# Kernel tuning notes

Hardware: AMD Instinct MI355X
Metric: run time of the kernel (lower is better)

Reference implementation:

```python
import jax, jax.numpy as jnp
import numpy as np

K = 4
TEMP = 0.5
PAD = 1

def setup_inputs() -> dict:
    key = jax.random.key(0)
    ks = jax.random.split(key, 5)
    B, C, H, W = 32, 256, 64, 64
    O, HID = 256, 65  # int(256*0.25)+1
    x = jax.random.normal(ks[0], (B, C, H, W), dtype=jnp.float32)
    w1 = jax.random.normal(ks[1], (HID, C), dtype=jnp.float32) * 0.05
    w2 = jax.random.normal(ks[2], (K * O, HID), dtype=jnp.float32) * 0.05
    b2 = jnp.zeros((K * O,), dtype=jnp.float32)
    weight = jax.random.normal(ks[3], (K, O, C, 3, 3), dtype=jnp.float32) * 0.05
    return {"x": x, "w1": w1, "w2": w2, "b2": b2, "weight": weight}

def _dyn_conv(x, w1, w2, b2, weight):
    B, C, H, W = x.shape
    Kk, O = weight.shape[0], weight.shape[1]
    # GPM2d attention: global avg pool -> 1x1 conv -> relu -> 1x1 conv -> softmax over K
    pooled = jnp.mean(x, axis=(2, 3))                     # [B, C]
    h = jax.nn.relu(pooled @ w1.T)                        # [B, HID]
    logits = (h @ w2.T + b2).reshape(B, Kk, O)            # [B, K, O]
    attn = jax.nn.softmax(logits / TEMP, axis=1)          # softmax over K experts
    # aggregate per-sample, per-out-channel weights: [B, O, C, k, k]
    agg_w = jnp.einsum('bko,kocij->bocij', attn, weight)
    # per-sample conv (equivalent to groups=batch trick in torch)
    def conv1(xi, wi):
        return jax.lax.conv_general_dilated(
            xi[None], wi, window_strides=(1, 1),
            padding=[(PAD, PAD), (PAD, PAD)],
            dimension_numbers=('NCHW', 'OIHW', 'NCHW'))[0]
    return jax.vmap(conv1)(x, agg_w)                      # [B, O, H, W]

def reference(x, w1, w2, b2, weight):
    return _dyn_conv(x, w1, w2, b2, weight)
```

## Files before the change

### kernel.cpp

```cpp
#include <hip/hip_runtime.h>
#include <stdint.h>

typedef unsigned short ushort_t;
typedef __attribute__((ext_vector_type(8))) short short8;
typedef __attribute__((ext_vector_type(8))) unsigned short ushortx8;
typedef __attribute__((ext_vector_type(4))) float floatx4;

#define B_    32
#define C_    256
#define O_    256
#define HID_  65
#define HW_   4096
#define KDIM  2304
#define XP_H  66
#define XPAD_ELEMS ((size_t)B_ * XP_H * XP_H * C_)
#define WAGG_ELEMS ((size_t)B_ * O_ * KDIM)

static __device__ __forceinline__ unsigned short f2bf(float f) {
  unsigned u = __float_as_uint(f);
  u += 0x7fffu + ((u >> 16) & 1u);
  return (unsigned short)(u >> 16);
}

static __device__ __forceinline__ void gld_lds16(const void* g, void* l) {
  __builtin_amdgcn_global_load_lds((__attribute__((address_space(1))) void*)(g),
                                   (__attribute__((address_space(3))) void*)(l),
                                   16, 0, 0);
}

__global__ void pad_kernel(const float* __restrict__ x, ushort_t* __restrict__ xpad,
                           float* __restrict__ partial) {
  __shared__ float tileT[64][65];
  __shared__ float pool[4][64];
  const int hwT = blockIdx.x, cT = blockIdx.y, b = blockIdx.z;
  const int t = threadIdx.x;
  const int hw0 = hwT * 64, c0 = cT * 64;
  const float* src = x + ((size_t)(b * C_ + c0)) * HW_ + hw0;

  if (cT == 0) {
    const int tid = hwT * 256 + t;
    if (tid < 8320) {
      uint4 z = {0u, 0u, 0u, 0u};
      uint4* base = (uint4*)(xpad + (size_t)b * XP_H * XP_H * C_);
      size_t idx;
      if (tid < 2112) idx = (size_t)tid;
      else if (tid < 4224) idx = (size_t)65 * 2112 + (tid - 2112);
      else if (tid < 6272) {
        const int i = tid - 4224;
        idx = (size_t)(1 + (i >> 5)) * 2112 + (i & 31);
      } else {
        const int i = tid - 6272;
        idx = (size_t)(1 + (i >> 5)) * 2112 + 65 * 32 + (i & 31);
      }
      base[idx] = z;
    }
  }

#pragma unroll
  for (int p = 0; p < 4; ++p) {
    const int flat = p * 256 + t;
    const int c = flat >> 4, h4 = (flat & 15) * 4;
    const float4 v = *(const float4*)(src + (size_t)c * HW_ + h4);
    tileT[h4 + 0][c] = v.x;
    tileT[h4 + 1][c] = v.y;
    tileT[h4 + 2][c] = v.z;
    tileT[h4 + 3][c] = v.w;
  }
  __syncthreads();

  {
    const int c = t & 63, qh = t >> 6;
    float s = 0.f;
#pragma unroll
    for (int i = 0; i < 16; ++i) s += tileT[qh * 16 + i][c];
    pool[qh][c] = s;
  }
  __syncthreads();
  if (t < 64) {
    partial[(size_t)hwT * (B_ * C_) + b * C_ + c0 + t] =
        pool[0][t] + pool[1][t] + pool[2][t] + pool[3][t];
  }

#pragma unroll
  for (int p = 0; p < 2; ++p) {
    const int flat = p * 256 + t;
    const int hw = flat >> 3, cg = (flat & 7) * 8;
    ushortx8 v;
#pragma unroll
    for (int j = 0; j < 8; ++j) v[j] = f2bf(tileT[hw][cg + j]);
    const int h = (hw0 + hw) >> 6, w = (hw0 + hw) & 63;
    *(ushortx8*)(xpad + (((size_t)b * XP_H + (h + 1)) * XP_H + (w + 1)) * C_ + c0 + cg) = v;
  }
}

__global__ void attn_kernel(const float* __restrict__ partial,
                            const float* __restrict__ w1,
                            const float* __restrict__ w2,
                            const float* __restrict__ b2,
                            float* __restrict__ attn) {
  __shared__ float sp[C_];
  __shared__ float sh[HID_];
  const int b = blockIdx.x, t = threadIdx.x;
  {
    float s = 0.f;
#pragma unroll
    for (int i = 0; i < 64; ++i) s += partial[(size_t)i * (B_ * C_) + b * C_ + t];
    sp[t] = s * (1.f / 4096.f);
  }
  __syncthreads();
  if (t < HID_) {
    float a = 0.f;
    for (int c = 0; c < C_; ++c) a += sp[c] * w1[t * C_ + c];
    sh[t] = fmaxf(a, 0.f);
  }
  __syncthreads();
  float lg[4];
#pragma unroll
  for (int k = 0; k < 4; ++k) {
    float a = b2[k * O_ + t];
    for (int j = 0; j < HID_; ++j) a += sh[j] * w2[(k * O_ + t) * HID_ + j];
    lg[k] = a * 2.0f;
  }
  float mx = fmaxf(fmaxf(lg[0], lg[1]), fmaxf(lg[2], lg[3]));
  float e0 = expf(lg[0] - mx), e1 = expf(lg[1] - mx);
  float e2 = expf(lg[2] - mx), e3 = expf(lg[3] - mx);
  float inv = 1.f / (e0 + e1 + e2 + e3);
  attn[(b * 4 + 0) * O_ + t] = e0 * inv;
  attn[(b * 4 + 1) * O_ + t] = e1 * inv;
  attn[(b * 4 + 2) * O_ + t] = e2 * inv;
  attn[(b * 4 + 3) * O_ + t] = e3 * inv;
}

__global__ void agg_kernel(const float* __restrict__ attn,
                           const float* __restrict__ wt,
                           ushort_t* __restrict__ wagg) {
  const int o = blockIdx.x;
  const int b0 = blockIdx.y * 4;
  const int t = threadIdx.x;
  float wr[4][9];
#pragma unroll
  for (int k = 0; k < 4; ++k) {
    const float* src = wt + (size_t)(k * O_ + o) * KDIM + t * 9;
#pragma unroll
    for (int n = 0; n < 9; ++n) wr[k][n] = src[n];
  }
#pragma unroll
  for (int bi = 0; bi < 4; ++bi) {
    const int b = b0 + bi;
    const float a0 = attn[(b * 4 + 0) * O_ + o];
    const float a1 = attn[(b * 4 + 1) * O_ + o];
    const float a2 = attn[(b * 4 + 2) * O_ + o];
    const float a3 = attn[(b * 4 + 3) * O_ + o];
    ushort_t* dst = wagg + (size_t)(b * O_ + o) * KDIM;
#pragma unroll
    for (int n = 0; n < 9; ++n) {
      float v = a0 * wr[0][n] + a1 * wr[1][n] + a2 * wr[2][n] + a3 * wr[3][n];
      dst[n * C_ + t] = f2bf(v);
    }
  }
}

__global__ __launch_bounds__(512) void gemm_kernel(const ushort_t* __restrict__ xpad,
                                                   const ushort_t* __restrict__ wagg,
                                                   float* __restrict__ out) {
  __shared__ short lA0[2 * 256 * 64];
  __shared__ short lB0[2 * 256 * 64];

  const int bid = blockIdx.x;
  const int xcd = bid & 7;
  const int q   = bid >> 3;
  const int b   = xcd + ((q >> 4) << 3);
  const int hwT = q & 15;
  const int hwBase = hwT << 8;
  const int h0     = hwT << 2;

  const int t    = threadIdx.x;
  const int lane = t & 63;
  const int wv   = t >> 6;

  const int rS  = lane >> 3;
  const int pS  = lane & 7;
  const int lch = pS ^ rS;
  size_t aG[4], bG[4];
  int ldsOff[4];
#pragma unroll
  for (int j = 0; j < 4; ++j) {
    const int row = wv * 32 + j * 8 + rS;
    aG[j] = (size_t)(b * O_ + row) * KDIM + lch * 8;
    const int hl = row >> 6, wl2 = row & 63;
    bG[j] = ((size_t)(b * XP_H + h0 + hl) * XP_H + wl2) * C_ + lch * 8;
    ldsOff[j] = (wv * 32 + j * 8) * 64;
  }

  const int lm   = lane & 15;
  const int quad = lane >> 4;
  const int wr   = wv >> 2;
  const int wc   = wv & 3;
  const int mW   = wr << 7;
  const int nW   = wc << 6;
  int aBase[2], bBase[2];
#pragma unroll
  for (int h = 0; h < 2; ++h) {
    const int ps = ((h * 4 + quad) ^ (lm & 7)) * 8;
    aBase[h] = (mW + lm) * 64 + ps;
    bBase[h] = (nW + lm) * 64 + ps;
  }

  floatx4 acc[8][4] = {};

#pragma unroll
  for (int j = 0; j < 4; ++j) {
    gld_lds16(wagg + aG[j], lA0 + ldsOff[j]);
    gld_lds16(xpad + bG[j], lB0 + ldsOff[j]);
  }
#pragma unroll
  for (int j = 0; j < 4; ++j) {
    gld_lds16(wagg + aG[j] + 64, lA0 + 16384 + ldsOff[j]);
    gld_lds16(xpad + bG[j] + 64, lB0 + 16384 + ldsOff[j]);
  }
  __builtin_amdgcn_s_waitcnt(0x0f78);
  __builtin_amdgcn_s_barrier();
  __builtin_amdgcn_sched_barrier(0);

#pragma unroll 1
  for (int tt = 0; tt < 36; ++tt) {
    const int cb = (tt & 1) * 16384;
    const short* bufA = lA0 + cb;
    const short* bufB = lB0 + cb;
#pragma unroll
    for (int h = 0; h < 2; ++h) {
      short8 af[8], bf[4];
#pragma unroll
      for (int i = 0; i < 8; ++i) af[i] = *(const short8*)(bufA + aBase[h] + i * 1024);
#pragma unroll
      for (int i = 0; i < 4; ++i) bf[i] = *(const short8*)(bufB + bBase[h] + i * 1024);
      __builtin_amdgcn_s_setprio(1);
#pragma unroll
      for (int mi = 0; mi < 8; ++mi)
#pragma unroll
        for (int ni = 0; ni < 4; ++ni)
          acc[mi][ni] = __builtin_amdgcn_mfma_f32_16x16x32_bf16(
              af[mi], bf[ni], acc[mi][ni], 0, 0, 0);
      __builtin_amdgcn_s_setprio(0);
    }
    if (tt == 35) break;
    __builtin_amdgcn_sched_barrier(0);
    __builtin_amdgcn_s_barrier();
    if (tt + 2 < 36) {
      const int kt  = tt + 2;
      const int tap = kt >> 2;
      const size_t aK = (size_t)kt << 6;
      const size_t bK = (size_t)((tap / 3) * XP_H + (tap % 3)) * C_ + ((kt & 3) << 6);
      short* dA = lA0 + cb;
      short* dB = lB0 + cb;
#pragma unroll
      for (int j = 0; j < 4; ++j) {
        gld_lds16(wagg + aG[j] + aK, dA + ldsOff[j]);
        gld_lds16(xpad + bG[j] + bK, dB + ldsOff[j]);
      }
      __builtin_amdgcn_s_waitcnt(0x0f78);
    } else {
      __builtin_amdgcn_s_waitcnt(0x0f70);
    }
    __builtin_amdgcn_s_barrier();
    __builtin_amdgcn_sched_barrier(0);
  }

  const size_t outBase = (size_t)b * O_ * HW_;
#pragma unroll
  for (int mi = 0; mi < 8; ++mi) {
#pragma unroll
    for (int ni = 0; ni < 4; ++ni) {
      const int hw = hwBase + nW + ni * 16 + lm;
#pragma unroll
      for (int r = 0; r < 4; ++r) {
        const int o = mW + mi * 16 + quad * 4 + r;
        out[outBase + (size_t)o * HW_ + hw] = acc[mi][ni][r];
      }
    }
  }
}

extern "C" void kernel_launch(void* const* d_in, const int* in_sizes, int n_in,
                              void* d_out, int out_size, void* d_ws, size_t ws_size,
                              hipStream_t stream) {
  const float* x  = (const float*)d_in[0];
  const float* w1 = (const float*)d_in[1];
  const float* w2 = (const float*)d_in[2];
  const float* b2 = (const float*)d_in[3];
  const float* wt = (const float*)d_in[4];
  float* out = (float*)d_out;

  char* ws = (char*)d_ws;
  ushort_t* xpad = (ushort_t*)ws;
  ushort_t* wagg = (ushort_t*)(ws + XPAD_ELEMS * 2);
  float* partial = (float*)(ws + XPAD_ELEMS * 2 + WAGG_ELEMS * 2);
  float* attn    = partial + 64 * B_ * C_;

  pad_kernel<<<dim3(64, 4, B_), 256, 0, stream>>>(x, xpad, partial);
  attn_kernel<<<B_, 256, 0, stream>>>(partial, w1, w2, b2, attn);
  agg_kernel<<<dim3(O_, 8), 256, 0, stream>>>(attn, wt, wagg);
  gemm_kernel<<<512, 512, 0, stream>>>(xpad, wagg, out);
}
```

Baseline: 428.5 us.

## Split main GEMM loop into four barrier-phased MFMA stages with staggered prefetch

Restructures the conv GEMM K-loop into four sub-phases, each loading half the A fragments from LDS and then running 16 MFMAs, with barriers between phases. Global-to-LDS loads for the next tiles are spread across phases: part of A for tt+1 early, the rest of A and all of B for tt+2 later. The staging row mapping is also remapped. The goal is to overlap LDS reads and global loads with MFMA work in a ping-pong style and to cut register pressure from 12 fragments to 8. The cost is many more barriers per iteration and more complex waitcnt accounting, which raises the risk of stalls or hazards.

```diff
diff --git a/kernel.cpp b/kernel.cpp
--- a/kernel.cpp
+++ b/kernel.cpp
@@ -27,6 +27,10 @@
                                    (__attribute__((address_space(3))) void*)(l),
                                    16, 0, 0);
 }
+
+#define FENCE() __builtin_amdgcn_sched_barrier(0)
+#define BAR()   __builtin_amdgcn_s_barrier()
+#define LGKM0() __builtin_amdgcn_s_waitcnt(0xC07F)
 
 __global__ void pad_kernel(const float* __restrict__ x, ushort_t* __restrict__ xpad,
                            float* __restrict__ partial) {
@@ -181,23 +185,20 @@
   const int rS  = lane >> 3;
   const int pS  = lane & 7;
   const int lch = pS ^ rS;
-  size_t aG[4], bG[4];
-  int ldsOff[4];
+  size_t aG2[4], bG2[4];
+  int sOff[4];
 #pragma unroll
   for (int j = 0; j < 4; ++j) {
-    const int row = wv * 32 + j * 8 + rS;
-    aG[j] = (size_t)(b * O_ + row) * KDIM + lch * 8;
-    const int hl = row >> 6, wl2 = row & 63;
-    bG[j] = ((size_t)(b * XP_H + h0 + hl) * XP_H + wl2) * C_ + lch * 8;
-    ldsOff[j] = (wv * 32 + j * 8) * 64;
+    const int row = j * 64 + wv * 8 + rS;
+    aG2[j] = (size_t)(b * O_ + row) * KDIM + lch * 8;
+    bG2[j] = ((size_t)(b * XP_H + h0 + j) * XP_H + (wv * 8 + rS)) * C_ + lch * 8;
+    sOff[j] = (j * 64 + wv * 8) * 64;
   }
 
   const int lm   = lane & 15;
   const int quad = lane >> 4;
-  const int wr   = wv >> 2;
-  const int wc   = wv & 3;
-  const int mW   = wr << 7;
-  const int nW   = wc << 6;
+  const int mW   = (wv >> 2) << 7;
+  const int nW   = (wv & 3) << 6;
   int aBase[2], bBase[2];
 #pragma unroll
   for (int h = 0; h < 2; ++h) {
@@ -206,64 +207,102 @@
     bBase[h] = (nW + lm) * 64 + ps;
   }
 
+  auto stageA = [&](int j, int kt, short* dst) {
+    gld_lds16(wagg + aG2[j] + ((size_t)kt << 6), dst + sOff[j]);
+  };
+  auto stageB = [&](int j, int kt, short* dst) {
+    const int tap = kt >> 2;
+    const size_t off = (size_t)((tap / 3) * XP_H + (tap % 3)) * C_ + ((kt & 3) << 6);
+    gld_lds16(xpad + bG2[j] + off, dst + sOff[j]);
+  };
+
   floatx4 acc[8][4] = {};
 
 #pragma unroll
   for (int j = 0; j < 4; ++j) {
-    gld_lds16(wagg + aG[j], lA0 + ldsOff[j]);
-    gld_lds16(xpad + bG[j], lB0 + ldsOff[j]);
-  }
-#pragma unroll
-  for (int j = 0; j < 4; ++j) {
-    gld_lds16(wagg + aG[j] + 64, lA0 + 16384 + ldsOff[j]);
-    gld_lds16(xpad + bG[j] + 64, lB0 + 16384 + ldsOff[j]);
-  }
-  __builtin_amdgcn_s_waitcnt(0x0f78);
-  __builtin_amdgcn_s_barrier();
-  __builtin_amdgcn_sched_barrier(0);
+    stageA(j, 0, lA0);
+    stageB(j, 0, lB0);
+  }
+  stageA(0, 1, lA0 + 16384);
+  stageA(2, 1, lA0 + 16384);
+#pragma unroll
+  for (int j = 0; j < 4; ++j) stageB(j, 1, lB0 + 16384);
+  __builtin_amdgcn_s_waitcnt(0x0f76);
+  BAR();
+  FENCE();
 
 #pragma unroll 1
   for (int tt = 0; tt < 36; ++tt) {
-    const int cb = (tt & 1) * 16384;
+    const int cb = (tt & 1) << 14;
     const short* bufA = lA0 + cb;
     const short* bufB = lB0 + cb;
-#pragma unroll
-    for (int h = 0; h < 2; ++h) {
-      short8 af[8], bf[4];
-#pragma unroll
-      for (int i = 0; i < 8; ++i) af[i] = *(const short8*)(bufA + aBase[h] + i * 1024);
-#pragma unroll
-      for (int i = 0; i < 4; ++i) bf[i] = *(const short8*)(bufB + bBase[h] + i * 1024);
-      __builtin_amdgcn_s_setprio(1);
-#pragma unroll
-      for (int mi = 0; mi < 8; ++mi)
-#pragma unroll
-        for (int ni = 0; ni < 4; ++ni)
-          acc[mi][ni] = __builtin_amdgcn_mfma_f32_16x16x32_bf16(
-              af[mi], bf[ni], acc[mi][ni], 0, 0, 0);
-      __builtin_amdgcn_s_setprio(0);
-    }
-    if (tt == 35) break;
-    __builtin_amdgcn_sched_barrier(0);
-    __builtin_amdgcn_s_barrier();
-    if (tt + 2 < 36) {
-      const int kt  = tt + 2;
-      const int tap = kt >> 2;
-      const size_t aK = (size_t)kt << 6;
-      const size_t bK = (size_t)((tap / 3) * XP_H + (tap % 3)) * C_ + ((kt & 3) << 6);
-      short* dA = lA0 + cb;
-      short* dB = lB0 + cb;
-#pragma unroll
-      for (int j = 0; j < 4; ++j) {
-        gld_lds16(wagg + aG[j] + aK, dA + ldsOff[j]);
-        gld_lds16(xpad + bG[j] + bK, dB + ldsOff[j]);
-      }
-      __builtin_amdgcn_s_waitcnt(0x0f78);
-    } else {
-      __builtin_amdgcn_s_waitcnt(0x0f70);
-    }
-    __builtin_amdgcn_s_barrier();
-    __builtin_amdgcn_sched_barrier(0);
+    short* oA = lA0 + (cb ^ 16384);
+    short8 af[4], bf[4];
+
+#pragma unroll
+    for (int i = 0; i < 4; ++i) af[i] = *(const short8*)(bufA + aBase[0] + i * 1024);
+#pragma unroll
+    for (int i = 0; i < 4; ++i) bf[i] = *(const short8*)(bufB + bBase[0] + i * 1024);
+    if (tt < 35) {
+      stageA(1, tt + 1, oA);
+      stageA(3, tt + 1, oA);
+    }
+    FENCE(); BAR(); LGKM0(); FENCE();
+    __builtin_amdgcn_s_setprio(1);
+#pragma unroll
+    for (int mi = 0; mi < 4; ++mi)
+#pragma unroll
+      for (int ni = 0; ni < 4; ++ni)
+        acc[mi][ni] = __builtin_amdgcn_mfma_f32_16x16x32_bf16(af[mi], bf[ni], acc[mi][ni], 0, 0, 0);
+    __builtin_amdgcn_s_setprio(0);
+    FENCE(); BAR(); FENCE();
+
+#pragma unroll
+    for (int i = 0; i < 4; ++i) af[i] = *(const short8*)(bufA + aBase[0] + (4 + i) * 1024);
+    FENCE(); BAR(); LGKM0(); FENCE();
+    __builtin_amdgcn_s_setprio(1);
+#pragma unroll
+    for (int mi = 0; mi < 4; ++mi)
+#pragma unroll
+      for (int ni = 0; ni < 4; ++ni)
+        acc[4 + mi][ni] = __builtin_amdgcn_mfma_f32_16x16x32_bf16(af[mi], bf[ni], acc[4 + mi][ni], 0, 0, 0);
+    __builtin_amdgcn_s_setprio(0);
+    FENCE(); BAR(); FENCE();
+
+#pragma unroll
+    for (int i = 0; i < 4; ++i) af[i] = *(const short8*)(bufA + aBase[1] + i * 1024);
+#pragma unroll
+    for (int i = 0; i < 4; ++i) bf[i] = *(const short8*)(bufB + bBase[1] + i * 1024);
+    FENCE(); BAR(); LGKM0(); FENCE();
+    __builtin_amdgcn_s_setprio(1);
+#pragma unroll
+    for (int mi = 0; mi < 4; ++mi)
+#pragma unroll
+      for (int ni = 0; ni < 4; ++ni)
+        acc[mi][ni] = __builtin_amdgcn_mfma_f32_16x16x32_bf16(af[mi], bf[ni], acc[mi][ni], 0, 0, 0);
+    __builtin_amdgcn_s_setprio(0);
+    FENCE(); BAR(); FENCE();
+
+#pragma unroll
+    for (int i = 0; i < 4; ++i) af[i] = *(const short8*)(bufA + aBase[1] + (4 + i) * 1024);
+    if (tt < 34) {
+      stageA(0, tt + 2, lA0 + cb);
+      stageA(2, tt + 2, lA0 + cb);
+#pragma unroll
+      for (int j = 0; j < 4; ++j) stageB(j, tt + 2, lB0 + cb);
+    }
+    FENCE(); BAR(); LGKM0(); FENCE();
+    __builtin_amdgcn_s_setprio(1);
+#pragma unroll
+    for (int mi = 0; mi < 4; ++mi)
+#pragma unroll
+      for (int ni = 0; ni < 4; ++ni)
+        acc[4 + mi][ni] = __builtin_amdgcn_mfma_f32_16x16x32_bf16(af[mi], bf[ni], acc[4 + mi][ni], 0, 0, 0);
+    __builtin_amdgcn_s_setprio(0);
+    FENCE();
+    if (tt < 34)      __builtin_amdgcn_s_waitcnt(0x0f76);
+    else if (tt == 34) __builtin_amdgcn_s_waitcnt(0x0f70);
+    if (tt < 35) { BAR(); FENCE(); }
   }
 
   const size_t outBase = (size_t)b * O_ * HW_;
```

Result: no change. 426.2 us (-0.5%).
